# Optimization experiments

Hardware: AMD Instinct MI355X
Metric: run time of the kernel (lower is better)

The kernel has to match this reference:

```python
import jax, jax.numpy as jnp
import numpy as np

RMS_EPS = 1e-5
L2_EPS = 1e-8


def _rms_norm(x, eps=RMS_EPS):
    return x * jax.lax.rsqrt(jnp.mean(x * x, axis=-1, keepdims=True) + eps)


def _l2_norm(x, eps=L2_EPS):
    return jnp.linalg.norm(x, ord=2, axis=-1, keepdims=True) + eps


def setup_inputs() -> dict:
    key = jax.random.key(0)
    kq, kk, kv = jax.random.split(key, 3)
    B, H, S, D = 4, 16, 4096, 64
    Q = jax.random.normal(kq, (B, H, S, D), dtype=jnp.float32)
    K = jax.random.normal(kk, (B, H, S, D), dtype=jnp.float32)
    V = jax.random.normal(kv, (B, H, S, D), dtype=jnp.float32)
    return {"Q": Q, "K": K, "V": V}


def reference(Q, K, V):
    # v_swiglu = SiLU(V) * V
    v_swiglu = jax.nn.silu(V) * V
    # causal cumulative sum over sequence dim
    c = jnp.cumsum(v_swiglu, axis=-2)
    c_n = _rms_norm(c)
    # gating scalar per (b,h,s): ||Q|| + ||K|| + 1
    r = _l2_norm(Q) + _l2_norm(K) + 1.0
    mstate = c_n / r
    # SwiGLU combine: V + SiLU(mstate) * V, then final RMSNorm
    out0 = V + jax.nn.silu(mstate) * V
    return _rms_norm(out0)
```

## Files before the change

kernel.cpp:

```cpp
#include <hip/hip_runtime.h>
#include <math.h>

#define BH 64
#define SEQ 4096
#define DIM 64
#define CHUNK 32
#define NCHUNK (SEQ / CHUNK)
#define WPB 4

__device__ __forceinline__ float fast_rcp(float x)  { return __builtin_amdgcn_rcpf(x); }
__device__ __forceinline__ float fast_rsqrt(float x){ return __builtin_amdgcn_rsqf(x); }

__device__ __forceinline__ float fast_sigmoid(float x) {
    return fast_rcp(1.0f + __expf(-x));
}

__global__ __launch_bounds__(256) void k_partials(const float* __restrict__ Q,
                                                  const float* __restrict__ K,
                                                  const float* __restrict__ V,
                                                  float* __restrict__ P,
                                                  float* __restrict__ R) {
    const int wave  = threadIdx.x >> 6;
    const int lane  = threadIdx.x & 63;
    const int chunk = blockIdx.x * WPB + wave;
    const size_t base = (size_t)chunk * (CHUNK * DIM) + lane;
    const float* qp = Q + base;
    const float* kp = K + base;
    const float* vp = V + base;

    float acc  = 0.0f;
    float my_r = 0.0f;
#pragma unroll 8
    for (int j = 0; j < CHUNK; ++j) {
        float q = qp[j * DIM];
        float k = kp[j * DIM];
        float v = vp[j * DIM];
        acc += v * v * fast_sigmoid(v);

        float q2 = q * q;
        float k2 = k * k;
#pragma unroll
        for (int m = 1; m < 64; m <<= 1) {
            q2 += __shfl_xor(q2, m);
            k2 += __shfl_xor(k2, m);
        }
        float r = sqrtf(q2) + sqrtf(k2) + 1.0f;
        if (lane == j) my_r = r;
    }
    P[(size_t)chunk * DIM + lane] = acc;
    if (lane < CHUNK) R[(size_t)chunk * CHUNK + lane] = my_r;
}

__global__ __launch_bounds__(64) void k_prefix(float* __restrict__ P) {
    const int bh   = blockIdx.x;
    const int lane = threadIdx.x;
    float* p = P + (size_t)bh * (NCHUNK * DIM) + lane;
    float run = 0.0f;
#pragma unroll 8
    for (int ck = 0; ck < NCHUNK; ++ck) {
        float t = p[ck * DIM];
        p[ck * DIM] = run;
        run += t;
    }
}

__global__ __launch_bounds__(256) void k_scan(const float* __restrict__ V,
                                              const float* __restrict__ P,
                                              const float* __restrict__ R,
                                              float* __restrict__ O) {
    const int wave  = threadIdx.x >> 6;
    const int lane  = threadIdx.x & 63;
    const int chunk = blockIdx.x * WPB + wave;
    const size_t base = (size_t)chunk * (CHUNK * DIM) + lane;
    const float* vp = V + base;
    float*       op = O + base;
    const float* rp = R + (size_t)chunk * CHUNK;

    float c = P[(size_t)chunk * DIM + lane];

#pragma unroll 8
    for (int j = 0; j < CHUNK; ++j) {
        float v = vp[j * DIM];
        float r = rp[j];

        float sw = v * v * fast_sigmoid(v);
        c += sw;

        float c2 = c * c;
#pragma unroll
        for (int m = 1; m < 64; m <<= 1) c2 += __shfl_xor(c2, m);

        float rms_c = fast_rsqrt(c2 * (1.0f / 64.0f) + 1e-5f);
        float m_    = c * rms_c * fast_rcp(r);
        float o     = v * (1.0f + m_ * fast_sigmoid(m_));

        float o2 = o * o;
#pragma unroll
        for (int m = 1; m < 64; m <<= 1) o2 += __shfl_xor(o2, m);

        op[j * DIM] = o * fast_rsqrt(o2 * (1.0f / 64.0f) + 1e-5f);
    }
}

extern "C" void kernel_launch(void* const* d_in, const int* in_sizes, int n_in,
                              void* d_out, int out_size, void* d_ws, size_t ws_size,
                              hipStream_t stream) {
    const float* Q = (const float*)d_in[0];
    const float* K = (const float*)d_in[1];
    const float* V = (const float*)d_in[2];
    float* O = (float*)d_out;
    float* P = (float*)d_ws;
    float* R = (float*)d_ws + (size_t)BH * NCHUNK * DIM;

    const int nchunks = BH * NCHUNK;
    k_partials<<<nchunks / WPB, 256, 0, stream>>>(Q, K, V, P, R);
    k_prefix<<<BH, 64, 0, stream>>>(P);
    k_scan<<<nchunks / WPB, 256, 0, stream>>>(V, P, R, O);
}
```

Before: 253.3 us.

## Vectorize partials and scan with float4 rows, parallelize chunk prefix across waves

```diff
diff --git a/kernel.cpp b/kernel.cpp
--- a/kernel.cpp
+++ b/kernel.cpp
@@ -10,10 +10,10 @@
 
 __device__ __forceinline__ float fast_rcp(float x)  { return __builtin_amdgcn_rcpf(x); }
 __device__ __forceinline__ float fast_rsqrt(float x){ return __builtin_amdgcn_rsqf(x); }
-
 __device__ __forceinline__ float fast_sigmoid(float x) {
     return fast_rcp(1.0f + __expf(-x));
 }
+
 
 __global__ __launch_bounds__(256) void k_partials(const float* __restrict__ Q,
                                                   const float* __restrict__ K,
@@ -22,46 +22,81 @@
                                                   float* __restrict__ R) {
     const int wave  = threadIdx.x >> 6;
     const int lane  = threadIdx.x & 63;
+    const int g     = lane >> 4;
+    const int h     = lane & 15;
     const int chunk = blockIdx.x * WPB + wave;
-    const size_t base = (size_t)chunk * (CHUNK * DIM) + lane;
-    const float* qp = Q + base;
-    const float* kp = K + base;
-    const float* vp = V + base;
 
-    float acc  = 0.0f;
-    float my_r = 0.0f;
-#pragma unroll 8
-    for (int j = 0; j < CHUNK; ++j) {
-        float q = qp[j * DIM];
-        float k = kp[j * DIM];
-        float v = vp[j * DIM];
-        acc += v * v * fast_sigmoid(v);
+    const size_t cbase = (size_t)chunk * (CHUNK * DIM);
+    const float4* q4 = (const float4*)(Q + cbase);
+    const float4* k4 = (const float4*)(K + cbase);
+    const float4* v4 = (const float4*)(V + cbase);
 
-        float q2 = q * q;
-        float k2 = k * k;
+    float acc0 = 0.f, acc1 = 0.f, acc2 = 0.f, acc3 = 0.f;
+
 #pragma unroll
-        for (int m = 1; m < 64; m <<= 1) {
+    for (int j0 = 0; j0 < CHUNK; j0 += 4) {
+        const int row = j0 + g;
+        const int idx = row * 16 + h;
+        float4 q = q4[idx];
+        float4 k = k4[idx];
+        float4 v = v4[idx];
+
+        float q2 = q.x*q.x + q.y*q.y + q.z*q.z + q.w*q.w;
+        float k2 = k.x*k.x + k.y*k.y + k.z*k.z + k.w*k.w;
+#pragma unroll
+        for (int m = 1; m < 16; m <<= 1) {
             q2 += __shfl_xor(q2, m);
             k2 += __shfl_xor(k2, m);
         }
         float r = sqrtf(q2) + sqrtf(k2) + 1.0f;
-        if (lane == j) my_r = r;
+        if (h == 0) R[(size_t)chunk * CHUNK + row] = r;
+
+        acc0 += v.x * v.x * fast_sigmoid(v.x);
+        acc1 += v.y * v.y * fast_sigmoid(v.y);
+        acc2 += v.z * v.z * fast_sigmoid(v.z);
+        acc3 += v.w * v.w * fast_sigmoid(v.w);
     }
-    P[(size_t)chunk * DIM + lane] = acc;
-    if (lane < CHUNK) R[(size_t)chunk * CHUNK + lane] = my_r;
+
+#pragma unroll
+    for (int m = 16; m < 64; m <<= 1) {
+        acc0 += __shfl_xor(acc0, m);
+        acc1 += __shfl_xor(acc1, m);
+        acc2 += __shfl_xor(acc2, m);
+        acc3 += __shfl_xor(acc3, m);
+    }
+    if (g == 0) {
+        float4 out = {acc0, acc1, acc2, acc3};
+        ((float4*)(P + (size_t)chunk * DIM))[h] = out;
+    }
 }
 
-__global__ __launch_bounds__(64) void k_prefix(float* __restrict__ P) {
+__global__ __launch_bounds__(256) void k_prefix(float* __restrict__ P) {
+    __shared__ float seg[WPB][DIM];
+    const int wave = threadIdx.x >> 6;
+    const int lane = threadIdx.x & 63;
     const int bh   = blockIdx.x;
-    const int lane = threadIdx.x;
-    float* p = P + (size_t)bh * (NCHUNK * DIM) + lane;
-    float run = 0.0f;
-#pragma unroll 8
-    for (int ck = 0; ck < NCHUNK; ++ck) {
-        float t = p[ck * DIM];
-        p[ck * DIM] = run;
-        run += t;
-    }
+    const int SEG  = NCHUNK / WPB;
+
+    float* p = P + (size_t)bh * (NCHUNK * DIM) + (size_t)wave * SEG * DIM + lane;
+
+    float t[SEG];
+#pragma unroll
+    for (int i = 0; i < SEG; ++i) t[i] = p[i * DIM];
+
+    float run = 0.f;
+#pragma unroll
+    for (int i = 0; i < SEG; ++i) { float x = t[i]; t[i] = run; run += x; }
+
+    seg[wave][lane] = run;
+    __syncthreads();
+
+    float carry = 0.f;
+#pragma unroll
+    for (int w = 0; w < WPB; ++w)
+        if (w < wave) carry += seg[w][lane];
+
+#pragma unroll
+    for (int i = 0; i < SEG; ++i) p[i * DIM] = t[i] + carry;
 }
 
 __global__ __launch_bounds__(256) void k_scan(const float* __restrict__ V,
@@ -70,35 +105,76 @@
                                               float* __restrict__ O) {
     const int wave  = threadIdx.x >> 6;
     const int lane  = threadIdx.x & 63;
+    const int g     = lane >> 4;
+    const int h     = lane & 15;
     const int chunk = blockIdx.x * WPB + wave;
-    const size_t base = (size_t)chunk * (CHUNK * DIM) + lane;
-    const float* vp = V + base;
-    float*       op = O + base;
-    const float* rp = R + (size_t)chunk * CHUNK;
 
-    float c = P[(size_t)chunk * DIM + lane];
+    const size_t cbase = (size_t)chunk * (CHUNK * DIM);
+    const float4* v4 = (const float4*)(V + cbase);
+    float4*       o4 = (float4*)(O + cbase);
+    const float*  rp = R + (size_t)chunk * CHUNK;
 
-#pragma unroll 8
-    for (int j = 0; j < CHUNK; ++j) {
-        float v = vp[j * DIM];
-        float r = rp[j];
+    float4 cb = ((const float4*)(P + (size_t)chunk * DIM))[h];
+    float c_base[4] = {cb.x, cb.y, cb.z, cb.w};
 
-        float sw = v * v * fast_sigmoid(v);
-        c += sw;
+    const int up16 = (lane + 48) & 63;
+    const int up32 = (lane + 32) & 63;
+    const int src3 = 48 + h;
 
-        float c2 = c * c;
 #pragma unroll
-        for (int m = 1; m < 64; m <<= 1) c2 += __shfl_xor(c2, m);
+    for (int j0 = 0; j0 < CHUNK; j0 += 4) {
+        const int row = j0 + g;
+        float4 v = v4[row * 16 + h];
 
+        float sw[4];
+        sw[0] = v.x * v.x * fast_sigmoid(v.x);
+        sw[1] = v.y * v.y * fast_sigmoid(v.y);
+        sw[2] = v.z * v.z * fast_sigmoid(v.z);
+        sw[3] = v.w * v.w * fast_sigmoid(v.w);
+
+#pragma unroll
+        for (int i = 0; i < 4; ++i) {
+            float t = __shfl(sw[i], up16);
+            sw[i] += (g >= 1) ? t : 0.f;
+        }
+#pragma unroll
+        for (int i = 0; i < 4; ++i) {
+            float t = __shfl(sw[i], up32);
+            sw[i] += (g >= 2) ? t : 0.f;
+        }
+
+        float c_row[4], tot[4];
+#pragma unroll
+        for (int i = 0; i < 4; ++i) {
+            tot[i]   = __shfl(sw[i], src3);
+            c_row[i] = c_base[i] + sw[i];
+            c_base[i] += tot[i];
+        }
+
+        float c2 = c_row[0]*c_row[0] + c_row[1]*c_row[1]
+                 + c_row[2]*c_row[2] + c_row[3]*c_row[3];
+#pragma unroll
+        for (int m = 1; m < 16; m <<= 1) c2 += __shfl_xor(c2, m);
+
+        float r     = rp[row];
         float rms_c = fast_rsqrt(c2 * (1.0f / 64.0f) + 1e-5f);
-        float m_    = c * rms_c * fast_rcp(r);
-        float o     = v * (1.0f + m_ * fast_sigmoid(m_));
+        float s     = rms_c * fast_rcp(r);
 
-        float o2 = o * o;
+        float vv[4] = {v.x, v.y, v.z, v.w};
+        float o[4];
 #pragma unroll
-        for (int m = 1; m < 64; m <<= 1) o2 += __shfl_xor(o2, m);
+        for (int i = 0; i < 4; ++i) {
+            float m_ = c_row[i] * s;
+            o[i] = vv[i] * (1.0f + m_ * fast_sigmoid(m_));
+        }
 
-        op[j * DIM] = o * fast_rsqrt(o2 * (1.0f / 64.0f) + 1e-5f);
+        float o2 = o[0]*o[0] + o[1]*o[1] + o[2]*o[2] + o[3]*o[3];
+#pragma unroll
+        for (int m = 1; m < 16; m <<= 1) o2 += __shfl_xor(o2, m);
+
+        float rms_o = fast_rsqrt(o2 * (1.0f / 64.0f) + 1e-5f);
+        float4 out = {o[0]*rms_o, o[1]*rms_o, o[2]*rms_o, o[3]*rms_o};
+        o4[row * 16 + h] = out;
     }
 }
 
@@ -114,6 +190,6 @@
 
     const int nchunks = BH * NCHUNK;
     k_partials<<<nchunks / WPB, 256, 0, stream>>>(Q, K, V, P, R);
-    k_prefix<<<BH, 64, 0, stream>>>(P);
+    k_prefix<<<BH, 256, 0, stream>>>(P);
     k_scan<<<nchunks / WPB, 256, 0, stream>>>(V, P, R, O);
 }
```

New measurement: 230.5 us. 1.1x faster.
